# Optimization experiments

Hardware: AMD Instinct MI355X
Metric: run time of the kernel (lower is better)

## Reference

```python
import jax, jax.numpy as jnp
import numpy as np

N_NODES = 100000
N_EDGES = 1600000
D_IN = 128
D_OUT = 32
DROP_P = 0.6
NEG_SLOPE = 0.2


def setup_inputs() -> dict:
    key = jax.random.key(0)
    ks = jax.random.split(key, 10)
    x = jax.random.normal(ks[0], (N_NODES, D_IN), dtype=jnp.float32)
    edge_index = jax.random.randint(ks[1], (2, N_EDGES), 0, N_NODES, dtype=jnp.int32)
    drop_u = jax.random.uniform(ks[2], (N_NODES, D_IN), dtype=jnp.float32)
    s = 1.0 / np.sqrt(D_IN)
    W_src = jax.random.normal(ks[3], (D_IN, D_OUT), dtype=jnp.float32) * s
    W_dst = jax.random.normal(ks[4], (D_IN, D_OUT), dtype=jnp.float32) * s
    att_src = jax.random.normal(ks[5], (D_OUT,), dtype=jnp.float32) * s
    att_dst = jax.random.normal(ks[6], (D_OUT,), dtype=jnp.float32) * s
    bias_gat = jax.random.normal(ks[7], (D_OUT,), dtype=jnp.float32) * 0.01
    W_lin = jax.random.normal(ks[8], (D_OUT, D_OUT), dtype=jnp.float32) / np.sqrt(D_OUT)
    b_lin = jax.random.normal(ks[9], (D_OUT,), dtype=jnp.float32) * 0.01
    return {"x": x, "edge_index": edge_index, "drop_u": drop_u,
            "W_src": W_src, "W_dst": W_dst, "att_src": att_src,
            "att_dst": att_dst, "bias_gat": bias_gat,
            "W_lin": W_lin, "b_lin": b_lin}


def reference(x, edge_index, drop_u, W_src, W_dst, att_src, att_dst,
              bias_gat, W_lin, b_lin):
    n = x.shape[0]
    # F.dropout(x, p=0.6, training=True) with deterministic uniform draws
    keep = (drop_u > DROP_P).astype(x.dtype)
    xd = x * keep / (1.0 - DROP_P)

    # GATConv (heads=1): separate src/dst linear maps
    h_src = xd @ W_src                      # [N, D_OUT]
    h_dst = xd @ W_dst                      # [N, D_OUT]
    a_src = h_src @ att_src                 # [N]
    a_dst = h_dst @ att_dst                 # [N]

    # add_self_loops=True (PyG default)
    loops = jnp.arange(n, dtype=edge_index.dtype)
    src = jnp.concatenate([edge_index[0], loops])   # [E+N]
    dst = jnp.concatenate([edge_index[1], loops])   # [E+N]

    e = a_src[src] + a_dst[dst]                      # per-edge raw score
    e = jnp.where(e > 0, e, NEG_SLOPE * e)           # leaky_relu(0.2)

    # segment softmax over destination-node neighborhoods
    e_max = jax.ops.segment_max(e, dst, num_segments=n)  # every node has a self loop
    e_exp = jnp.exp(e - e_max[dst])
    denom = jax.ops.segment_sum(e_exp, dst, num_segments=n)
    alpha = e_exp / denom[dst]                       # [E+N]

    # scatter-add aggregation of weighted source features
    msg = h_src[src] * alpha[:, None]                # [E+N, D_OUT]
    out = jax.ops.segment_sum(msg, dst, num_segments=n) + bias_gat

    # residual linear + relu + log_softmax
    out = out + out @ W_lin + b_lin
    out = jax.nn.relu(out)
    logp = jax.nn.log_softmax(out, axis=1)
    return logp, alpha
```

## Files before the change

kernel.cpp:

```cpp
#include <hip/hip_runtime.h>
#include <hip/hip_bf16.h>
#include <math.h>

#define D_IN   128
#define D_OUT  32
#define NEG_SLOPE 0.2f
#define DROP_P 0.6f
#define KEEP_SCALE 2.5f

#define NPB     64
#define NB      1563
#define NBPAD   2048
#define CAPB    1536
#define CHUNK   2048
#define BT      512
#define EPT     4
#define SRC_BITS 17
#define SRC_MASK ((1u << SRC_BITS) - 1)
#define EPT3    6

typedef __attribute__((ext_vector_type(8))) short fragAB;
typedef __attribute__((ext_vector_type(4))) float fragCD;

__device__ __forceinline__ void atomicMaxF(float* addr, float v) {
    if (v >= 0.0f) atomicMax((int*)addr, __float_as_int(v));
    else           atomicMin((unsigned int*)addr, __float_as_uint(v));
}

__device__ __forceinline__ unsigned pack_bf16(float lo, float hi) {
    __hip_bfloat16 l = __float2bfloat16(lo);
    __hip_bfloat16 h = __float2bfloat16(hi);
    unsigned short lb, hb;
    __builtin_memcpy(&lb, &l, 2);
    __builtin_memcpy(&hb, &h, 2);
    return (unsigned)lb | ((unsigned)hb << 16);
}

__device__ __forceinline__ unsigned short f2bf(float f) {
    __hip_bfloat16 h = __float2bfloat16(f);
    unsigned short u;
    __builtin_memcpy(&u, &h, 2);
    return u;
}

__global__ void k_fold(const float* __restrict__ W_src, const float* __restrict__ W_dst,
                       const float* __restrict__ att_src, const float* __restrict__ att_dst,
                       float* __restrict__ v_src, float* __restrict__ v_dst,
                       int* __restrict__ gcur, uint4* __restrict__ wfrag) {
    int gi = blockIdx.x * blockDim.x + threadIdx.x;
    if (gi < NB) gcur[gi] = gi * CAPB;
    if (gi < 512) {
        int tile = gi >> 8;
        int kb   = (gi >> 6) & 3;
        int lane = gi & 63;
        int grp = lane >> 4, col = lane & 15;
        int kbase = kb * 32 + grp * 8;
        int cidx  = tile * 16 + col;
        unsigned o0 = pack_bf16(W_src[(kbase + 0) * D_OUT + cidx], W_src[(kbase + 1) * D_OUT + cidx]);
        unsigned o1 = pack_bf16(W_src[(kbase + 2) * D_OUT + cidx], W_src[(kbase + 3) * D_OUT + cidx]);
        unsigned o2 = pack_bf16(W_src[(kbase + 4) * D_OUT + cidx], W_src[(kbase + 5) * D_OUT + cidx]);
        unsigned o3 = pack_bf16(W_src[(kbase + 6) * D_OUT + cidx], W_src[(kbase + 7) * D_OUT + cidx]);
        wfrag[gi] = make_uint4(o0, o1, o2, o3);
    }
    if (blockIdx.x == 0) {
        int k = threadIdx.x;
        if (k < D_IN) {
            float s = 0.f, d = 0.f;
            #pragma unroll
            for (int c = 0; c < D_OUT; ++c) {
                s += W_src[k * D_OUT + c] * att_src[c];
                d += W_dst[k * D_OUT + c] * att_dst[c];
            }
            v_src[k] = s;
            v_dst[k] = d;
        }
    }
}

__global__ __launch_bounds__(256) void k_nodes_mfma(
    const float* __restrict__ x, const float* __restrict__ drop_u,
    const uint4* __restrict__ wfrag,
    const float* __restrict__ v_src, const float* __restrict__ v_dst,
    unsigned short* __restrict__ h_bf16,
    float* __restrict__ a_src, float* __restrict__ a_dst,
    int n)
{
    int tid  = threadIdx.x;
    int wv   = tid >> 6;
    int lane = tid & 63;
    int nbase = blockIdx.x * 64 + wv * 16;
    int row = lane & 15, grp = lane >> 4;

    int arow_raw = nbase + row;
    bool aact = arow_raw < n;
    int arow = aact ? arow_raw : (n - 1);
    const float* xr = x      + (size_t)arow * D_IN;
    const float* dr = drop_u + (size_t)arow * D_IN;

    fragCD c0 = {0.f, 0.f, 0.f, 0.f};
    fragCD c1 = {0.f, 0.f, 0.f, 0.f};
    float ps = 0.f, pd = 0.f;

    #pragma unroll
    for (int kb = 0; kb < 4; ++kb) {
        int k0 = kb * 32 + grp * 8;
        float4 xa = *(const float4*)(xr + k0);
        float4 xb = *(const float4*)(xr + k0 + 4);
        float4 da = *(const float4*)(dr + k0);
        float4 db = *(const float4*)(dr + k0 + 4);
        float f0 = da.x > DROP_P ? xa.x * KEEP_SCALE : 0.f;
        float f1 = da.y > DROP_P ? xa.y * KEEP_SCALE : 0.f;
        float f2 = da.z > DROP_P ? xa.z * KEEP_SCALE : 0.f;
        float f3 = da.w > DROP_P ? xa.w * KEEP_SCALE : 0.f;
        float f4 = db.x > DROP_P ? xb.x * KEEP_SCALE : 0.f;
        float f5 = db.y > DROP_P ? xb.y * KEEP_SCALE : 0.f;
        float f6 = db.z > DROP_P ? xb.z * KEEP_SCALE : 0.f;
        float f7 = db.w > DROP_P ? xb.w * KEEP_SCALE : 0.f;

        float4 vs1 = *(const float4*)(v_src + k0);
        float4 vs2 = *(const float4*)(v_src + k0 + 4);
        float4 vd1 = *(const float4*)(v_dst + k0);
        float4 vd2 = *(const float4*)(v_dst + k0 + 4);
        ps += f0 * vs1.x + f1 * vs1.y + f2 * vs1.z + f3 * vs1.w
            + f4 * vs2.x + f5 * vs2.y + f6 * vs2.z + f7 * vs2.w;
        pd += f0 * vd1.x + f1 * vd1.y + f2 * vd1.z + f3 * vd1.w
            + f4 * vd2.x + f5 * vd2.y + f6 * vd2.z + f7 * vd2.w;

        union { unsigned u[4]; fragAB v; } af;
        af.u[0] = pack_bf16(f0, f1);
        af.u[1] = pack_bf16(f2, f3);
        af.u[2] = pack_bf16(f4, f5);
        af.u[3] = pack_bf16(f6, f7);

        fragAB b0 = *reinterpret_cast<const fragAB*>(&wfrag[kb * 64 + lane]);
        fragAB b1 = *reinterpret_cast<const fragAB*>(&wfrag[256 + kb * 64 + lane]);
        c0 = __builtin_amdgcn_mfma_f32_16x16x32_bf16(af.v, b0, c0, 0, 0, 0);
        c1 = __builtin_amdgcn_mfma_f32_16x16x32_bf16(af.v, b1, c1, 0, 0, 0);
    }

    ps += __shfl_xor(ps, 16); ps += __shfl_xor(ps, 32);
    pd += __shfl_xor(pd, 16); pd += __shfl_xor(pd, 32);
    if (grp == 0 && aact) { a_src[arow_raw] = ps; a_dst[arow_raw] = pd; }

    #pragma unroll
    for (int r = 0; r < 4; ++r) {
        int onode = nbase + grp * 4 + r;
        if (onode < n) {
            h_bf16[(size_t)onode * D_OUT + row]      = f2bf(c0[r]);
            h_bf16[(size_t)onode * D_OUT + 16 + row] = f2bf(c1[r]);
        }
    }
}

__global__ __launch_bounds__(256) void k_nodes(
    const float* __restrict__ x, const float* __restrict__ drop_u,
    const float* __restrict__ W_src,
    const float* __restrict__ v_src, const float* __restrict__ v_dst,
    float* __restrict__ h_src, float* __restrict__ a_src, float* __restrict__ a_dst,
    float* __restrict__ e_max, float* __restrict__ denom,
    float* __restrict__ agg, int n, int init_aux)
{
    int gt = blockIdx.x * 256 + threadIdx.x;
    int node_raw = gt >> 2;
    int sub = gt & 3;
    bool act = node_raw < n;
    int node = act ? node_raw : (n - 1);

    const float4* xr4 = (const float4*)(x      + (size_t)node * D_IN) + sub * 8;
    const float4* dr4 = (const float4*)(drop_u + (size_t)node * D_IN) + sub * 8;
    const float*  wb  = W_src + sub * 32 * D_OUT;
    const float4* vsp = (const float4*)v_src + sub * 8;
    const float4* vdp = (const float4*)v_dst + sub * 8;

    float4 xv[8];
    #pragma unroll
    for (int q = 0; q < 8; ++q) {
        float4 xl = xr4[q];
        float4 dl = dr4[q];
        xv[q].x = dl.x > DROP_P ? xl.x * KEEP_SCALE : 0.f;
        xv[q].y = dl.y > DROP_P ? xl.y * KEEP_SCALE : 0.f;
        xv[q].z = dl.z > DROP_P ? xl.z * KEEP_SCALE : 0.f;
        xv[q].w = dl.w > DROP_P ? xl.w * KEEP_SCALE : 0.f;
    }

    float acc[D_OUT];
    #pragma unroll
    for (int c = 0; c < D_OUT; ++c) acc[c] = 0.f;
    float ps = 0.f, pd = 0.f;

    #pragma unroll
    for (int q = 0; q < 8; ++q) {
        float4 vs4 = vsp[q];
        float4 vd4 = vdp[q];
        ps += xv[q].x * vs4.x + xv[q].y * vs4.y + xv[q].z * vs4.z + xv[q].w * vs4.w;
        pd += xv[q].x * vd4.x + xv[q].y * vd4.y + xv[q].z * vd4.z + xv[q].w * vd4.w;
        #pragma unroll
        for (int kk = 0; kk < 4; ++kk) {
            float xk = (kk == 0) ? xv[q].x : (kk == 1) ? xv[q].y : (kk == 2) ? xv[q].z : xv[q].w;
            const float4* wrow = (const float4*)(wb + (q * 4 + kk) * D_OUT);
            #pragma unroll
            for (int c4 = 0; c4 < 8; ++c4) {
                float4 w = wrow[c4];
                acc[c4 * 4 + 0] += xk * w.x;
                acc[c4 * 4 + 1] += xk * w.y;
                acc[c4 * 4 + 2] += xk * w.z;
                acc[c4 * 4 + 3] += xk * w.w;
            }
        }
    }

    #pragma unroll
    for (int c = 0; c < D_OUT; ++c) {
        acc[c] += __shfl_xor(acc[c], 1);
        acc[c] += __shfl_xor(acc[c], 2);
    }
    ps += __shfl_xor(ps, 1); ps += __shfl_xor(ps, 2);
    pd += __shfl_xor(pd, 1); pd += __shfl_xor(pd, 2);

    if (act) {
        if (sub == 0) {
            a_src[node] = ps;
            a_dst[node] = pd;
            if (init_aux) { e_max[node] = -3.0e38f; denom[node] = 0.f; }
        }
        float o[8];
        if (sub == 0) {
            #pragma unroll
            for (int i = 0; i < 8; ++i) o[i] = acc[i];
        } else if (sub == 1) {
            #pragma unroll
            for (int i = 0; i < 8; ++i) o[i] = acc[8 + i];
        } else if (sub == 2) {
            #pragma unroll
            for (int i = 0; i < 8; ++i) o[i] = acc[16 + i];
        } else {
            #pragma unroll
            for (int i = 0; i < 8; ++i) o[i] = acc[24 + i];
        }
        float4* hb = (float4*)(h_src + (size_t)node * D_OUT + sub * 8);
        hb[0] = make_float4(o[0], o[1], o[2], o[3]);
        hb[1] = make_float4(o[4], o[5], o[6], o[7]);
        if (init_aux) {
            float4* ab = (float4*)(agg + (size_t)node * D_OUT + sub * 8);
            ab[0] = make_float4(0.f, 0.f, 0.f, 0.f);
            ab[1] = make_float4(0.f, 0.f, 0.f, 0.f);
        }
    }
}

__global__ __launch_bounds__(BT) void k_binsort(
    const int* __restrict__ ei, int E, int n,
    const float* __restrict__ a_src, const float* __restrict__ a_dst,
    int* __restrict__ gcur, uint2* __restrict__ binned)
{
    __shared__ int A[NBPAD], B[NBPAD];
    __shared__ int excl[NB + 1];
    __shared__ int lcur[NB];
    __shared__ int gpos[NB];
    __shared__ uint2 stage[CHUNK];
    __shared__ unsigned short sbk[CHUNK];

    int tid = threadIdx.x;
    int T   = E + n;
    int base = blockIdx.x * CHUNK;

    for (int k = tid; k < NBPAD; k += BT) A[k] = 0;
    __syncthreads();

    uint2 rec[EPT];
    int   bk [EPT];
    #pragma unroll
    for (int e = 0; e < EPT; ++e) {
        int i = base + e * BT + tid;
        if (i < T) {
            int s, d;
            if (i < E) { s = ei[i]; d = ei[E + i]; }
            else       { s = d = i - E; }
            int b    = d >> 6;
            int drel = d & 63;
            float sc = a_src[s] + a_dst[d];
            sc = sc > 0.f ? sc : NEG_SLOPE * sc;
            rec[e].x = (unsigned)s | ((unsigned)drel << SRC_BITS);
            rec[e].y = __float_as_uint(expf(sc));
            bk[e]  = b;
            atomicAdd(&A[b], 1);
        } else bk[e] = -1;
    }
    __syncthreads();

    int* cur = A; int* nxt = B;
    for (int off = 1; off < NBPAD; off <<= 1) {
        for (int k = tid; k < NBPAD; k += BT) {
            int v = cur[k];
            if (k >= off) v += cur[k - off];
            nxt[k] = v;
        }
        __syncthreads();
        int* t = cur; cur = nxt; nxt = t;
    }

    for (int b = tid; b < NB; b += BT) {
        int e0 = b ? cur[b - 1] : 0;
        excl[b] = e0;
        lcur[b] = e0;
        int c = cur[b] - e0;
        gpos[b] = c ? atomicAdd(&gcur[b], c) : 0;
    }
    if (tid == 0) excl[NB] = cur[NB - 1];
    __syncthreads();

    #pragma unroll
    for (int e = 0; e < EPT; ++e) {
        if (bk[e] >= 0) {
            int slot = atomicAdd(&lcur[bk[e]], 1);
            stage[slot] = rec[e];
            sbk[slot]   = (unsigned short)bk[e];
        }
    }
    __syncthreads();

    int tot = excl[NB];
    for (int j = tid; j < tot; j += BT) {
        int b = sbk[j];
        unsigned gd = (unsigned)(gpos[b] + (j - excl[b]));
        if (gd < (unsigned)(b + 1) * CAPB)
            binned[gd] = stage[j];
    }
}

__global__ __launch_bounds__(256) void k_bucket4(
    const uint2* __restrict__ binned, const int* __restrict__ gcur,
    const unsigned short* __restrict__ h_bf16,
    const float* __restrict__ bias_gat, const float* __restrict__ W_lin,
    const float* __restrict__ b_lin,
    float* __restrict__ inv_out,
    float* __restrict__ io, int n)
{
    __shared__ uint2 grp[CAPB];
    __shared__ int A[NPB];
    __shared__ int ends[NPB];
    __shared__ int ncur[NPB];
    __shared__ float Wl[D_OUT * D_OUT];
    __shared__ float ul[8][D_OUT];

    int tid = threadIdx.x;
    int b   = blockIdx.x;
    int n0  = b * NPB;
    int nn  = n - n0; if (nn > NPB) nn = NPB;
    if (nn <= 0) return;

    for (int i = tid; i < D_OUT * D_OUT; i += 256) Wl[i] = W_lin[i];
    if (tid < NPB) A[tid] = 0;
    __syncthreads();

    int cnt = gcur[b] - b * CAPB;
    if (cnt > CAPB) cnt = CAPB;
    const uint2* src = binned + (size_t)b * CAPB;

    uint2 rr[EPT3];
    #pragma unroll
    for (int e = 0; e < EPT3; ++e) {
        int j = tid + e * 256;
        if (j < cnt) {
            uint2 r = src[j];
            rr[e] = r;
            atomicAdd(&A[r.x >> SRC_BITS], 1);
        }
    }
    __syncthreads();

    if (tid < NPB) {
        int v = A[tid];
        #pragma unroll
        for (int off = 1; off < NPB; off <<= 1) {
            int u = __shfl_up(v, off);
            if (tid >= off) v += u;
        }
        ends[tid] = v;
        ncur[tid] = v - A[tid];
    }
    __syncthreads();

    #pragma unroll
    for (int e = 0; e < EPT3; ++e) {
        int j = tid + e * 256;
        if (j < cnt) {
            uint2 r = rr[e];
            int pos = atomicAdd(&ncur[r.x >> SRC_BITS], 1);
            grp[pos] = make_uint2(r.x & SRC_MASK, r.y);
        }
    }
    __syncthreads();

    int g = tid >> 5, lane = tid & 31;
    float bg = bias_gat[lane];
    float bl = b_lin[lane];

    for (int nr = g; nr < nn; nr += 8) {
        int st = nr ? ends[nr - 1] : 0;
        int en = ends[nr];
        int node = n0 + nr;

        float ss = 0.f;
        for (int j = st + lane; j < en; j += 32)
            ss += __uint_as_float(grp[j].y);
        #pragma unroll
        for (int o = 16; o; o >>= 1) ss += __shfl_xor(ss, o);
        float inv = 1.0f / ss;
        if (lane == 0) inv_out[node] = inv;

        float acc0 = 0.f, acc1 = 0.f, acc2 = 0.f, acc3 = 0.f;
        float acc4 = 0.f, acc5 = 0.f, acc6 = 0.f, acc7 = 0.f;
        int j = st;
        for (; j + 7 < en; j += 8) {
            uint2 p0 = grp[j],     p1 = grp[j + 1];
            uint2 p2 = grp[j + 2], p3 = grp[j + 3];
            uint2 p4 = grp[j + 4], p5 = grp[j + 5];
            uint2 p6 = grp[j + 6], p7 = grp[j + 7];
            float h0 = __uint_as_float((unsigned)h_bf16[(p0.x << 5) + lane] << 16);
            float h1 = __uint_as_float((unsigned)h_bf16[(p1.x << 5) + lane] << 16);
            float h2 = __uint_as_float((unsigned)h_bf16[(p2.x << 5) + lane] << 16);
            float h3 = __uint_as_float((unsigned)h_bf16[(p3.x << 5) + lane] << 16);
            float h4 = __uint_as_float((unsigned)h_bf16[(p4.x << 5) + lane] << 16);
            float h5 = __uint_as_float((unsigned)h_bf16[(p5.x << 5) + lane] << 16);
            float h6 = __uint_as_float((unsigned)h_bf16[(p6.x << 5) + lane] << 16);
            float h7 = __uint_as_float((unsigned)h_bf16[(p7.x << 5) + lane] << 16);
            acc0 += h0 * __uint_as_float(p0.y);
            acc1 += h1 * __uint_as_float(p1.y);
            acc2 += h2 * __uint_as_float(p2.y);
            acc3 += h3 * __uint_as_float(p3.y);
            acc4 += h4 * __uint_as_float(p4.y);
            acc5 += h5 * __uint_as_float(p5.y);
            acc6 += h6 * __uint_as_float(p6.y);
            acc7 += h7 * __uint_as_float(p7.y);
        }
        for (; j < en; ++j) {
            uint2 p = grp[j];
            acc0 += __uint_as_float((unsigned)h_bf16[(p.x << 5) + lane] << 16)
                  * __uint_as_float(p.y);
        }

        float u = (((acc0 + acc1) + (acc2 + acc3)) + ((acc4 + acc5) + (acc6 + acc7))) * inv + bg;
        ul[g][lane] = u;
        float r2 = u + bl;
        #pragma unroll 8
        for (int k = 0; k < D_OUT; ++k)
            r2 += ul[g][k] * Wl[k * D_OUT + lane];
        r2 = fmaxf(r2, 0.f);

        float mm = r2;
        #pragma unroll
        for (int o = 16; o; o >>= 1) mm = fmaxf(mm, __shfl_xor(mm, o));
        float e2 = expf(r2 - mm);
        float s2 = e2;
        #pragma unroll
        for (int o = 16; o; o >>= 1) s2 += __shfl_xor(s2, o);
        io[(size_t)node * D_OUT + lane] = r2 - mm - logf(s2);
    }
}

__global__ void k_alpha(const int* __restrict__ ei, int E, int n,
                        const float* __restrict__ a_src, const float* __restrict__ a_dst,
                        const float* __restrict__ inv,
                        float* __restrict__ alpha_out)
{
    int i = blockIdx.x * blockDim.x + threadIdx.x;
    int T = E + n;
    if (i >= T) return;
    int s, d;
    if (i < E) { s = ei[i]; d = ei[E + i]; }
    else       { s = d = i - E; }
    float e = a_src[s] + a_dst[d];
    e = e > 0.f ? e : NEG_SLOPE * e;
    alpha_out[i] = expf(e) * inv[d];
}

__global__ void k_edge_score(const int* __restrict__ ei, int E, int n,
                             const float* __restrict__ a_src, const float* __restrict__ a_dst,
                             float* __restrict__ score_out, float* __restrict__ e_max)
{
    int total = E + n;
    int i = blockIdx.x * blockDim.x + threadIdx.x;
    if (i >= total) return;
    int s, d;
    if (i < E) { s = ei[i]; d = ei[E + i]; }
    else       { s = d = i - E; }
    float e = a_src[s] + a_dst[d];
    e = e > 0.f ? e : NEG_SLOPE * e;
    score_out[i] = e;
    atomicMaxF(&e_max[d], e);
}

__global__ void k_edge_exp(const int* __restrict__ ei, int E, int n,
                           const float* __restrict__ e_max,
                           float* __restrict__ score_io, float* __restrict__ denom)
{
    int total = E + n;
    int i = blockIdx.x * blockDim.x + threadIdx.x;
    if (i >= total) return;
    int d = (i < E) ? ei[E + i] : (i - E);
    float ex = expf(score_io[i] - e_max[d]);
    score_io[i] = ex;
    atomicAdd(&denom[d], ex);
}

__global__ __launch_bounds__(256) void k_edge_agg(
    const int* __restrict__ ei, int E, int n,
    const float* __restrict__ h_src, const float* __restrict__ denom,
    float* __restrict__ alpha_io, float* __restrict__ agg)
{
    int tid  = threadIdx.x;
    int loc  = tid >> 5;
    int lane = tid & 31;
    int i = blockIdx.x * 8 + loc;
    int total = E + n;
    if (i >= total) return;
    int s, d;
    if (i < E) { s = ei[i]; d = ei[E + i]; }
    else       { s = d = i - E; }
    float alpha = alpha_io[i] / denom[d];
    if (lane == 0) alpha_io[i] = alpha;
    float m = h_src[(size_t)s * D_OUT + lane] * alpha;
    atomicAdd(&agg[(size_t)d * D_OUT + lane], m);
}

__global__ __launch_bounds__(256) void k_final(
    const float* __restrict__ bias_gat, const float* __restrict__ W_lin,
    const float* __restrict__ b_lin, float* __restrict__ io, int n)
{
    __shared__ float Wl[D_OUT * D_OUT];
    __shared__ float ul[8][D_OUT];

    int tid = threadIdx.x;
    for (int i = tid; i < D_OUT * D_OUT; i += 256) Wl[i] = W_lin[i];
    __syncthreads();

    int loc  = tid >> 5;
    int lane = tid & 31;
    int node = blockIdx.x * 8 + loc;

    float u = 0.f;
    if (node < n) u = io[(size_t)node * D_OUT + lane] + bias_gat[lane];
    ul[loc][lane] = u;
    __syncthreads();

    float r = u + b_lin[lane];
    #pragma unroll 8
    for (int k = 0; k < D_OUT; ++k)
        r += ul[loc][k] * Wl[k * D_OUT + lane];
    r = fmaxf(r, 0.f);

    float m = r;
    #pragma unroll
    for (int off = 16; off; off >>= 1) m = fmaxf(m, __shfl_xor(m, off));
    float ex = expf(r - m);
    float ssum = ex;
    #pragma unroll
    for (int off = 16; off; off >>= 1) ssum += __shfl_xor(ssum, off);
    float logp = r - m - logf(ssum);

    if (node < n) io[(size_t)node * D_OUT + lane] = logp;
}

extern "C" void kernel_launch(void* const* d_in, const int* in_sizes, int n_in,
                              void* d_out, int out_size, void* d_ws, size_t ws_size,
                              hipStream_t stream)
{
    const float* x        = (const float*)d_in[0];
    const int*   ei       = (const int*)  d_in[1];
    const float* drop_u   = (const float*)d_in[2];
    const float* W_src    = (const float*)d_in[3];
    const float* W_dst    = (const float*)d_in[4];
    const float* att_src  = (const float*)d_in[5];
    const float* att_dst  = (const float*)d_in[6];
    const float* bias_gat = (const float*)d_in[7];
    const float* W_lin    = (const float*)d_in[8];
    const float* b_lin    = (const float*)d_in[9];

    const int N = in_sizes[0] / D_IN;
    const int E = in_sizes[1] / 2;
    const int total = E + N;

    float* ws = (float*)d_ws;

    float* v_src = ws;
    float* v_dst = ws + 128;
    float* h_src = ws + 256;
    unsigned short* h_bf16 = (unsigned short*)h_src;
    float* a_src = h_src + (size_t)N * D_OUT;
    float* a_dst = a_src + N;
    float* m_buf = a_dst + N;
    float* i_buf = m_buf + N;

    size_t idx = 256 + (size_t)N * D_OUT + 4 * (size_t)N;
    int* gcur = (int*)(ws + idx);       idx += NB + 2;
    idx = (idx + 3) & ~(size_t)3;
    uint4* wfrag = (uint4*)(ws + idx);  idx += 2048;
    uint2* binned = (uint2*)(ws + idx); idx += 2 * (size_t)NB * CAPB;
    size_t need_bytes = idx * sizeof(float);

    float* logp_out  = (float*)d_out;
    float* alpha_out = (float*)d_out + (size_t)N * D_OUT;

    int mfmaBlocks = (N + 63) / 64;
    int nodeBlocks = (int)(((size_t)N * 4 + 255) / 256);
    int nodeBlocks8 = (N + 7) / 8;
    int eb = (total + 255) / 256;

    bool fits = (ws_size >= need_bytes) && (N < (1 << SRC_BITS)) && (N <= NB * NPB);

    if (fits) {
        k_fold<<<(NB + 127) / 128, 128, 0, stream>>>(W_src, W_dst, att_src, att_dst,
                                                     v_src, v_dst, gcur, wfrag);
        k_nodes_mfma<<<mfmaBlocks, 256, 0, stream>>>(x, drop_u, wfrag, v_src, v_dst,
                                                     h_bf16, a_src, a_dst, N);
        int nchunk = (total + CHUNK - 1) / CHUNK;
        k_binsort<<<nchunk, BT, 0, stream>>>(ei, E, N, a_src, a_dst, gcur, binned);
        k_bucket4<<<NB, 256, 0, stream>>>(binned, gcur, h_bf16,
                                          bias_gat, W_lin, b_lin,
                                          i_buf, logp_out, N);
        k_alpha<<<eb, 256, 0, stream>>>(ei, E, N, a_src, a_dst, i_buf, alpha_out);
    } else {
        k_fold<<<(NB + 127) / 128, 128, 0, stream>>>(W_src, W_dst, att_src, att_dst,
                                                     v_src, v_dst, gcur, wfrag);
        k_nodes<<<nodeBlocks, 256, 0, stream>>>(x, drop_u, W_src, v_src, v_dst,
                                                h_src, a_src, a_dst,
                                                m_buf, i_buf, logp_out, N, 1);
        k_edge_score<<<eb, 256, 0, stream>>>(ei, E, N, a_src, a_dst, alpha_out, m_buf);
        k_edge_exp<<<eb, 256, 0, stream>>>(ei, E, N, m_buf, alpha_out, i_buf);
        int aggBlocks = (total + 7) / 8;
        k_edge_agg<<<aggBlocks, 256, 0, stream>>>(ei, E, N, h_src, i_buf, alpha_out, logp_out);
        k_final<<<nodeBlocks8, 256, 0, stream>>>(bias_gat, W_lin, b_lin, logp_out, N);
    }
}
```

Measured before the change: 145.4 us.

## Double destination-bucket size and replace Hillis-Steele scan with wave-shuffle scan

Buckets now cover 128 destination nodes instead of 64, halving the bucket count and the per-chunk histogram. The binsort kernel drops from 512 to 256 threads with 8 edges per thread. Its multi-pass shared-memory Hillis-Steele prefix scan becomes a per-thread 4-element sum plus a wavefront shuffle scan, which cuts the barrier count. The bucket kernel runs with 512 threads and 16 node groups and uses a two-wave scan over 128 node counters. Larger buckets mean fewer global atomics and scattered writes, at the cost of more shared memory per block, and any bucket holding more than 2816 edges would be silently truncated.

After: 140.8 us. 3.1% less time.

```diff
diff --git a/kernel.cpp b/kernel.cpp
--- a/kernel.cpp
+++ b/kernel.cpp
@@ -8,16 +8,17 @@
 #define DROP_P 0.6f
 #define KEEP_SCALE 2.5f
 
-#define NPB     64
-#define NB      1563
-#define NBPAD   2048
-#define CAPB    1536
+#define NPB     128
+#define NB      782
+#define NBPAD   1024
+#define CAPB    2816
 #define CHUNK   2048
-#define BT      512
-#define EPT     4
+#define BT      256
+#define EPT     8
 #define SRC_BITS 17
 #define SRC_MASK ((1u << SRC_BITS) - 1)
-#define EPT3    6
+#define BT5     512
+#define EPT5    6
 
 typedef __attribute__((ext_vector_type(8))) short fragAB;
 typedef __attribute__((ext_vector_type(4))) float fragCD;
@@ -248,15 +249,15 @@
     }
 }
 
-__global__ __launch_bounds__(BT) void k_binsort(
+__global__ __launch_bounds__(BT) void k_binsort2(
     const int* __restrict__ ei, int E, int n,
     const float* __restrict__ a_src, const float* __restrict__ a_dst,
     int* __restrict__ gcur, uint2* __restrict__ binned)
 {
-    __shared__ int A[NBPAD], B[NBPAD];
-    __shared__ int excl[NB + 1];
+    __shared__ int A[NBPAD];
     __shared__ int lcur[NB];
     __shared__ int gpos[NB];
+    __shared__ int wsum[4];
     __shared__ uint2 stage[CHUNK];
     __shared__ unsigned short sbk[CHUNK];
 
@@ -264,6 +265,7 @@
     int T   = E + n;
     int base = blockIdx.x * CHUNK;
 
+    #pragma unroll
     for (int k = tid; k < NBPAD; k += BT) A[k] = 0;
     __syncthreads();
 
@@ -276,8 +278,8 @@
             int s, d;
             if (i < E) { s = ei[i]; d = ei[E + i]; }
             else       { s = d = i - E; }
-            int b    = d >> 6;
-            int drel = d & 63;
+            int b    = d >> 7;
+            int drel = d & 127;
             float sc = a_src[s] + a_dst[d];
             sc = sc > 0.f ? sc : NEG_SLOPE * sc;
             rec[e].x = (unsigned)s | ((unsigned)drel << SRC_BITS);
@@ -288,25 +290,34 @@
     }
     __syncthreads();
 
-    int* cur = A; int* nxt = B;
-    for (int off = 1; off < NBPAD; off <<= 1) {
-        for (int k = tid; k < NBPAD; k += BT) {
-            int v = cur[k];
-            if (k >= off) v += cur[k - off];
-            nxt[k] = v;
-        }
-        __syncthreads();
-        int* t = cur; cur = nxt; nxt = t;
-    }
+    int a0 = A[4 * tid], a1 = A[4 * tid + 1], a2 = A[4 * tid + 2], a3 = A[4 * tid + 3];
+    int s4 = a0 + a1 + a2 + a3;
+    int incl = s4;
+    int lane = tid & 63, wv = tid >> 6;
+    #pragma unroll
+    for (int off = 1; off < 64; off <<= 1) {
+        int u = __shfl_up(incl, off);
+        if (lane >= off) incl += u;
+    }
+    if (lane == 63) wsum[wv] = incl;
+    __syncthreads();
+    int wexcl = 0;
+    #pragma unroll
+    for (int w = 0; w < 4; ++w)
+        if (w < wv) wexcl += wsum[w];
+    int bse = wexcl + incl - s4;
+    A[4 * tid]     = bse + a0;
+    A[4 * tid + 1] = bse + a0 + a1;
+    A[4 * tid + 2] = bse + a0 + a1 + a2;
+    A[4 * tid + 3] = bse + s4;
+    __syncthreads();
 
     for (int b = tid; b < NB; b += BT) {
-        int e0 = b ? cur[b - 1] : 0;
-        excl[b] = e0;
+        int e0 = b ? A[b - 1] : 0;
+        int c  = A[b] - e0;
         lcur[b] = e0;
-        int c = cur[b] - e0;
         gpos[b] = c ? atomicAdd(&gcur[b], c) : 0;
     }
-    if (tid == 0) excl[NB] = cur[NB - 1];
     __syncthreads();
 
     #pragma unroll
@@ -319,16 +330,17 @@
     }
     __syncthreads();
 
-    int tot = excl[NB];
+    int tot = A[NBPAD - 1];
     for (int j = tid; j < tot; j += BT) {
         int b = sbk[j];
-        unsigned gd = (unsigned)(gpos[b] + (j - excl[b]));
+        int e0 = b ? A[b - 1] : 0;
+        unsigned gd = (unsigned)(gpos[b] + (j - e0));
         if (gd < (unsigned)(b + 1) * CAPB)
             binned[gd] = stage[j];
     }
 }
 
-__global__ __launch_bounds__(256) void k_bucket4(
+__global__ __launch_bounds__(BT5) void k_bucket5(
     const uint2* __restrict__ binned, const int* __restrict__ gcur,
     const unsigned short* __restrict__ h_bf16,
     const float* __restrict__ bias_gat, const float* __restrict__ W_lin,
@@ -340,8 +352,9 @@
     __shared__ int A[NPB];
     __shared__ int ends[NPB];
     __shared__ int ncur[NPB];
+    __shared__ int wtot0;
     __shared__ float Wl[D_OUT * D_OUT];
-    __shared__ float ul[8][D_OUT];
+    __shared__ float ul[16][D_OUT];
 
     int tid = threadIdx.x;
     int b   = blockIdx.x;
@@ -349,7 +362,7 @@
     int nn  = n - n0; if (nn > NPB) nn = NPB;
     if (nn <= 0) return;
 
-    for (int i = tid; i < D_OUT * D_OUT; i += 256) Wl[i] = W_lin[i];
+    for (int i = tid; i < D_OUT * D_OUT; i += BT5) Wl[i] = W_lin[i];
     if (tid < NPB) A[tid] = 0;
     __syncthreads();
 
@@ -357,10 +370,10 @@
     if (cnt > CAPB) cnt = CAPB;
     const uint2* src = binned + (size_t)b * CAPB;
 
-    uint2 rr[EPT3];
-    #pragma unroll
-    for (int e = 0; e < EPT3; ++e) {
-        int j = tid + e * 256;
+    uint2 rr[EPT5];
+    #pragma unroll
+    for (int e = 0; e < EPT5; ++e) {
+        int j = tid + e * BT5;
         if (j < cnt) {
             uint2 r = src[j];
             rr[e] = r;
@@ -369,21 +382,25 @@
     }
     __syncthreads();
 
+    int c0 = 0, v = 0;
+    if (tid < NPB) { c0 = A[tid]; v = c0; }
     if (tid < NPB) {
-        int v = A[tid];
+        int lane = tid & 63;
         #pragma unroll
-        for (int off = 1; off < NPB; off <<= 1) {
+        for (int off = 1; off < 64; off <<= 1) {
             int u = __shfl_up(v, off);
-            if (tid >= off) v += u;
-        }
-        ends[tid] = v;
-        ncur[tid] = v - A[tid];
-    }
-    __syncthreads();
-
-    #pragma unroll
-    for (int e = 0; e < EPT3; ++e) {
-        int j = tid + e * 256;
+            if (lane >= off) v += u;
+        }
+    }
+    if (tid == 63) wtot0 = v;
+    __syncthreads();
+    if (tid >= 64 && tid < NPB) v += wtot0;
+    if (tid < NPB) { ends[tid] = v; ncur[tid] = v - c0; }
+    __syncthreads();
+
+    #pragma unroll
+    for (int e = 0; e < EPT5; ++e) {
+        int j = tid + e * BT5;
         if (j < cnt) {
             uint2 r = rr[e];
             int pos = atomicAdd(&ncur[r.x >> SRC_BITS], 1);
@@ -396,7 +413,7 @@
     float bg = bias_gat[lane];
     float bl = b_lin[lane];
 
-    for (int nr = g; nr < nn; nr += 8) {
+    for (int nr = g; nr < nn; nr += 16) {
         int st = nr ? ends[nr - 1] : 0;
         int en = ends[nr];
         int node = n0 + nr;
@@ -615,8 +632,8 @@
         k_nodes_mfma<<<mfmaBlocks, 256, 0, stream>>>(x, drop_u, wfrag, v_src, v_dst,
                                                      h_bf16, a_src, a_dst, N);
         int nchunk = (total + CHUNK - 1) / CHUNK;
-        k_binsort<<<nchunk, BT, 0, stream>>>(ei, E, N, a_src, a_dst, gcur, binned);
-        k_bucket4<<<NB, 256, 0, stream>>>(binned, gcur, h_bf16,
+        k_binsort2<<<nchunk, BT, 0, stream>>>(ei, E, N, a_src, a_dst, gcur, binned);
+        k_bucket5<<<NB, BT5, 0, stream>>>(binned, gcur, h_bf16,
                                           bias_gat, W_lin, b_lin,
                                           i_buf, logp_out, N);
         k_alpha<<<eb, 256, 0, stream>>>(ei, E, N, a_src, a_dst, i_buf, alpha_out);
```
